# Optimization experiments

Measured on AMD Instinct MI355X. Metric: run time of the kernel, lower is better.

The kernel has to match this reference:

```python
import jax, jax.numpy as jnp
import numpy as np

B, C, L = 4, 512, 4096
H = 8
DH = C // H
MLP = 2048


def _ln(x, g, b, eps=1e-5):
    mu = x.mean(-1, keepdims=True)
    var = ((x - mu) ** 2).mean(-1, keepdims=True)
    return (x - mu) / jnp.sqrt(var + eps) * g + b


def setup_inputs() -> dict:
    key = jax.random.key(0)
    ks = jax.random.split(key, 16)
    s = 0.02
    d = {
        "x": jax.random.normal(ks[0], (B, C, L), jnp.float32),
        "Wq": jax.random.normal(ks[1], (C, C), jnp.float32) * s,
        "bq": jnp.zeros((C,), jnp.float32),
        "gq": jnp.ones((C,), jnp.float32),
        "betaq": jnp.zeros((C,), jnp.float32),
        "Wk": jax.random.normal(ks[2], (C, C), jnp.float32) * s,
        "bk": jnp.zeros((C,), jnp.float32),
        "gk": jnp.ones((C,), jnp.float32),
        "betak": jnp.zeros((C,), jnp.float32),
        "Wv": jax.random.normal(ks[3], (C, C), jnp.float32) * s,
        "bv": jnp.zeros((C,), jnp.float32),
        "gv": jnp.ones((C,), jnp.float32),
        "betav": jnp.zeros((C,), jnp.float32),
        "Wkq": jax.random.normal(ks[4], (C, C), jnp.float32) * s,
        "bkq": jnp.zeros((C,), jnp.float32),
        "Wkk": jax.random.normal(ks[5], (C, C), jnp.float32) * s,
        "bkk": jnp.zeros((C,), jnp.float32),
        "g_attn": jnp.ones((C,), jnp.float32),
        "b_attn": jnp.zeros((C,), jnp.float32),
        "W1": jax.random.normal(ks[6], (C, MLP), jnp.float32) * s,
        "b1": jnp.zeros((MLP,), jnp.float32),
        "W2": jax.random.normal(ks[7], (MLP, C), jnp.float32) * s,
        "b2": jnp.zeros((C,), jnp.float32),
    }
    return d


def _split_heads(t):
    # [B, L, C] -> [B, H, L, DH]
    b, l, _ = t.shape
    return t.reshape(b, l, H, DH).transpose(0, 2, 1, 3)


def reference(x, Wq, bq, gq, betaq, Wk, bk, gk, betak, Wv, bv, gv, betav,
              Wkq, bkq, Wkk, bkk, g_attn, b_attn, W1, b1, W2, b2):
    # x: [B, C, L] -> flatten(2).permute(0,2,1) -> [B, L, C]
    xf = jnp.transpose(x, (0, 2, 1))
    Q = _ln(xf @ Wq + bq, gq, betaq)            # [B, L, C]
    K = _ln(xf @ Wk + bk, gk, betak)            # [B, L, C]
    V = _ln(xf @ Wv + bv, gv, betav)            # [B, L, C]
    # add zero token to K, V (seq dim)
    z = jnp.zeros((x.shape[0], 1, C), x.dtype)
    K = jnp.concatenate([z, K], axis=1)         # [B, Lk, C], Lk = L+1
    V = jnp.concatenate([z, V], axis=1)
    phiQ = jnp.tanh(Q @ Wkq + bkq) + 1.0        # [B, L, C]
    phiK = jnp.tanh(K @ Wkk + bkk) + 1.0        # [B, Lk, C]

    Qh, Kh, Vh = _split_heads(Q), _split_heads(K), _split_heads(V)
    pQ, pK = _split_heads(phiQ), _split_heads(phiK)  # [B,H,L,DH], [B,H,Lk,DH]

    # softmax-reweighted phi_K: score from mean-query probe against K
    q_probe = Qh.mean(axis=2)                                   # [B,H,DH]
    score = jnp.einsum('bhd,bhld->bhl', q_probe, Kh) / jnp.sqrt(jnp.float32(DH))
    score = jax.nn.softmax(score, axis=-1)                      # [B,H,Lk]
    pKw = pK * score[..., None]                                 # [B,H,Lk,DH]

    kv = jnp.einsum('bhld,bhle->bhde', pKw, Vh)                 # [B,H,DH,DH]
    num = jnp.einsum('bhqd,bhde->bhqe', pQ, kv)                 # [B,H,L,DH]
    ksum = pKw.sum(axis=2)                                      # [B,H,DH]
    bottom = jnp.einsum('bhqd,bhd->bhq', pQ, ksum)[..., None] + 1e-6
    out_h = num / bottom                                        # [B,H,L,DH]

    out = out_h.transpose(0, 2, 1, 3).reshape(x.shape[0], -1, C)  # [B,L,C]
    a = _ln(out, g_attn, b_attn)
    m = jax.nn.gelu(a @ W1 + b1, approximate=False) @ W2 + b2
    res = a + m                                                 # residual MLP
    res = jnp.transpose(res, (0, 2, 1))                         # [B,C,L]
    return res + x
```

## Files before the change

kernel.cpp:

```cpp
#include <hip/hip_runtime.h>
#include <math.h>

#define B_ 4
#define C_ 512
#define L_ 4096
#define H_ 8
#define DH_ 64
#define MLP_ 2048
#define BL_ (B_*L_)
#define LK_ (L_+1)

typedef _Float16 f16;
typedef _Float16 f16x8 __attribute__((ext_vector_type(8)));
typedef _Float16 f16x4 __attribute__((ext_vector_type(4)));
typedef float f32x4 __attribute__((ext_vector_type(4)));

__device__ __forceinline__ void gl16(void* lds, const void* g) {
  __builtin_amdgcn_global_load_lds((const __attribute__((address_space(1))) void*)g,
                                   (__attribute__((address_space(3))) void*)lds,
                                   16, 0, 0);
}

__device__ __forceinline__ float frcp(float x) { return __builtin_amdgcn_rcpf(x); }

__global__ __launch_bounds__(256) void transpose_w(const float* __restrict__ W,
                                                   f16* __restrict__ Wt, int K, int N) {
  __shared__ float tile[32][33];
  int n0 = blockIdx.x * 32, k0 = blockIdx.y * 32;
  int tx = threadIdx.x & 31, ty = threadIdx.x >> 5;
#pragma unroll
  for (int i = 0; i < 4; ++i)
    tile[ty + i * 8][tx] = W[(size_t)(k0 + ty + i * 8) * N + n0 + tx];
  __syncthreads();
#pragma unroll
  for (int i = 0; i < 4; ++i)
    Wt[(size_t)(n0 + ty + i * 8) * K + k0 + tx] = (f16)tile[tx][ty + i * 8];
}

__global__ __launch_bounds__(256) void transpose_x(const float* __restrict__ x,
                                                   f16* __restrict__ xf) {
  __shared__ float tile[32][33];
  int b = blockIdx.z;
  int l0 = blockIdx.x * 32, c0 = blockIdx.y * 32;
  int tx = threadIdx.x & 31, ty = threadIdx.x >> 5;
#pragma unroll
  for (int i = 0; i < 4; ++i)
    tile[ty + i * 8][tx] = x[((size_t)b * C_ + c0 + ty + i * 8) * L_ + l0 + tx];
  __syncthreads();
#pragma unroll
  for (int i = 0; i < 4; ++i)
    xf[((size_t)b * L_ + l0 + ty + i * 8) * C_ + c0 + tx] = (f16)tile[tx][ty + i * 8];
}

__global__ __launch_bounds__(256) void final_add(const f16* __restrict__ a,
                                                 const f16* __restrict__ m,
                                                 const float* __restrict__ x,
                                                 float* __restrict__ out) {
  __shared__ float tile[32][33];
  int b = blockIdx.z;
  int l0 = blockIdx.x * 32, c0 = blockIdx.y * 32;
  int tx = threadIdx.x & 31, ty = threadIdx.x >> 5;
#pragma unroll
  for (int i = 0; i < 4; ++i) {
    size_t idx = ((size_t)b * L_ + l0 + ty + i * 8) * C_ + c0 + tx;
    tile[ty + i * 8][tx] = (float)a[idx] + (float)m[idx];
  }
  __syncthreads();
#pragma unroll
  for (int i = 0; i < 4; ++i) {
    size_t o = ((size_t)b * C_ + c0 + ty + i * 8) * L_ + l0 + tx;
    out[o] = tile[tx][ty + i * 8] + x[o];
  }
}

__global__ __launch_bounds__(256) void pack_params(
    const float* bq, const float* bk, const float* bv,
    const float* gq, const float* gk, const float* gv,
    const float* betaq, const float* betak, const float* betav,
    const float* bkq, const float* bkk,
    float* bqkv, float* gqkv, float* betaqkv, float* bphi) {
  int i = blockIdx.x * 256 + threadIdx.x;
  int w = i >> 9, c = i & 511;
  bqkv[i]    = (w == 0 ? bq : (w == 1 ? bk : bv))[c];
  gqkv[i]    = (w == 0 ? gq : (w == 1 ? gk : gv))[c];
  betaqkv[i] = (w == 0 ? betaq : (w == 1 ? betak : betav))[c];
  if (i < 1024) bphi[i] = (i < 512) ? bkq[i] : bkk[i - 512];
}

template <int EPI>
__global__ __launch_bounds__(256) void gemm64(const f16* __restrict__ A,
                                              const f16* __restrict__ Bt,
                                              const float* __restrict__ bias,
                                              f16* __restrict__ Ch,
                                              int N, int K,
                                              const float* __restrict__ Bot,
                                              long long zA, long long zB,
                                              long long zC, long long zBias,
                                              long long zBot) {
  __shared__ f16 smem[2 * 128 * 64];
  f16* As = smem;
  f16* Bs = smem + 128 * 64;
  A  += (size_t)blockIdx.z * zA;
  Bt += (size_t)blockIdx.z * zB;
  Ch += (size_t)blockIdx.z * zC;
  if (EPI == 3) Bot += (size_t)blockIdx.z * zBot;
  else          bias += (size_t)blockIdx.z * zBias;

  const int tid = threadIdx.x;
  const int lane = tid & 63, wv = tid >> 6;
  const int wm = wv >> 1, wn = wv & 1;
  const int bm = blockIdx.x * 128, bn = blockIdx.y * 128;
  const int l15 = lane & 15, q = lane >> 4;

  const int srow = tid >> 3;
  const int schunk = (tid & 7) ^ (srow & 7);
  const f16* pa = A + (size_t)(bm + srow) * K + schunk * 8;
  const f16* pb = Bt + (size_t)(bn + srow) * K + schunk * 8;
  f16* la = As + tid * 8;
  f16* lb = Bs + tid * 8;
  const int sw0 = (q ^ (lane & 7)) * 8;
  const int sw1 = ((4 + q) ^ (lane & 7)) * 8;

  f32x4 acc[4][4] = {};

  for (int k0 = 0; k0 < K; k0 += 64) {
    __syncthreads();
#pragma unroll
    for (int p = 0; p < 4; ++p) gl16(la + p * 2048, pa + (size_t)p * 32 * K + k0);
#pragma unroll
    for (int p = 0; p < 4; ++p) gl16(lb + p * 2048, pb + (size_t)p * 32 * K + k0);
    __syncthreads();
#pragma unroll
    for (int ks = 0; ks < 2; ++ks) {
      const int sw = ks ? sw1 : sw0;
      f16x8 af[4], bf[4];
#pragma unroll
      for (int i = 0; i < 4; ++i)
        af[i] = *(const f16x8*)&As[(wm * 64 + i * 16 + l15) * 64 + sw];
#pragma unroll
      for (int j = 0; j < 4; ++j)
        bf[j] = *(const f16x8*)&Bs[(wn * 64 + j * 16 + l15) * 64 + sw];
#pragma unroll
      for (int i = 0; i < 4; ++i)
#pragma unroll
        for (int j = 0; j < 4; ++j)
          acc[i][j] = __builtin_amdgcn_mfma_f32_16x16x32_f16(af[i], bf[j], acc[i][j], 0, 0, 0);
    }
  }

  __syncthreads();
#pragma unroll
  for (int j = 0; j < 4; ++j) {
    int lc = wn * 64 + j * 16 + l15;
    float bb = (EPI == 3) ? 0.f : bias[bn + lc];
#pragma unroll
    for (int i = 0; i < 4; ++i) {
#pragma unroll
      for (int r = 0; r < 4; ++r) {
        int lr = wm * 64 + i * 16 + q * 4 + r;
        float v = acc[i][j][r] + bb;
        if (EPI == 1) {
          v = 2.0f * frcp(1.0f + __expf(-2.0f * v));
        } else if (EPI == 2) {
          v = v * frcp(1.0f + __expf(-1.5957691f * (v + 0.044715f * v * v * v)));
        } else if (EPI == 3) {
          v = v * frcp(Bot[(size_t)(bm + lr) * H_ + ((bn + lc) >> 6)] + 1e-6f);
        }
        smem[lr * 128 + ((((lc >> 3) ^ (lr & 15)) << 3) | (lc & 7))] = (f16)v;
      }
    }
  }
  __syncthreads();
#pragma unroll
  for (int p = 0; p < 8; ++p) {
    int idx = p * 256 + tid;
    int row = idx >> 4, ch = idx & 15;
    f16x8 vv = *(const f16x8*)&smem[row * 128 + ((ch ^ (row & 15)) << 3)];
    *(f16x8*)&Ch[(size_t)(bm + row) * N + bn + ch * 8] = vv;
  }
}

__global__ __launch_bounds__(256) void ln16(const f16* __restrict__ X,
                                            const float* __restrict__ g,
                                            const float* __restrict__ bta,
                                            f16* __restrict__ Y, int threeway) {
  int wv = threadIdx.x >> 6, lane = threadIdx.x & 63;
  int r = blockIdx.x * 4 + wv;
  int token = r, which = 0;
  if (threeway) { token = r / 3; which = r - token * 3; }
  const f16* xr = X + (size_t)r * C_;
  f16x8 v = *(const f16x8*)(xr + lane * 8);
  float vals[8];
  float s = 0.f, s2 = 0.f;
#pragma unroll
  for (int j = 0; j < 8; ++j) { vals[j] = (float)v[j]; s += vals[j]; s2 += vals[j] * vals[j]; }
#pragma unroll
  for (int m_ = 1; m_ < 64; m_ <<= 1) { s += __shfl_xor(s, m_); s2 += __shfl_xor(s2, m_); }
  float mu = s * (1.f / C_);
  float var = s2 * (1.f / C_) - mu * mu;
  float rstd = rsqrtf(var + 1e-5f);
  const float* gp = g + which * C_;
  const float* bp = bta + which * C_;
  f16x8 o;
#pragma unroll
  for (int j = 0; j < 8; ++j) {
    int c = lane * 8 + j;
    o[j] = (f16)((vals[j] - mu) * rstd * gp[c] + bp[c]);
  }
  *(f16x8*)(Y + ((size_t)which * BL_ + token) * C_ + lane * 8) = o;
}

__global__ __launch_bounds__(256) void qprobe2(const f16* __restrict__ Q,
                                               float* __restrict__ qp) {
  int blk = blockIdx.x;
  int b = blk >> 6;
  int r0 = blk * 64;
  int t = threadIdx.x;
  int c8 = (t & 63) * 8, rg = t >> 6;
  float s[8] = {0.f, 0.f, 0.f, 0.f, 0.f, 0.f, 0.f, 0.f};
#pragma unroll
  for (int i = 0; i < 16; ++i) {
    const f16* row = Q + ((size_t)r0 + rg + i * 4) * C_ + c8;
    f16x8 v = *(const f16x8*)row;
#pragma unroll
    for (int j = 0; j < 8; ++j) s[j] += (float)v[j];
  }
  __shared__ float red[4][520];
#pragma unroll
  for (int j = 0; j < 8; ++j) red[rg][c8 + j] = s[j];
  __syncthreads();
  int c = t * 2;
  float a0 = red[0][c] + red[1][c] + red[2][c] + red[3][c];
  float a1 = red[0][c + 1] + red[1][c + 1] + red[2][c + 1] + red[3][c + 1];
  atomicAdd(&qp[b * C_ + c], a0);
  atomicAdd(&qp[b * C_ + c + 1], a1);
}

__global__ __launch_bounds__(256) void logits_kernel(const f16* __restrict__ Kh,
                                                     const float* __restrict__ qp,
                                                     float* __restrict__ score) {
  int wv = threadIdx.x >> 6, lane = threadIdx.x & 63;
  int token = blockIdx.x * 4 + wv;
  int b = token >> 12;
  int l = token & (L_ - 1);
  const f16* row = Kh + (size_t)token * C_;
  int h = lane >> 3, j0 = (lane & 7) * 8;
  const float* qph = qp + b * C_ + h * DH_ + j0;
  float p = 0.f;
#pragma unroll
  for (int j = 0; j < 8; ++j) p += qph[j] * (float)row[h * DH_ + j0 + j];
  p += __shfl_xor(p, 1); p += __shfl_xor(p, 2); p += __shfl_xor(p, 4);
  if ((lane & 7) == 0)
    score[((size_t)b * H_ + h) * LK_ + 1 + l] = p * (1.f / L_) * 0.125f;
}

__global__ __launch_bounds__(256) void softmax_kernel(float* __restrict__ score) {
  int bh = blockIdx.x, t = threadIdx.x;
  float* s = score + (size_t)bh * LK_;
  __shared__ float red[256];
  float mx = 0.f;
  for (int i = t; i < L_; i += 256) mx = fmaxf(mx, s[1 + i]);
  red[t] = mx; __syncthreads();
  for (int k = 128; k; k >>= 1) { if (t < k) red[t] = fmaxf(red[t], red[t + k]); __syncthreads(); }
  mx = red[0]; __syncthreads();
  float sum = (t == 0) ? expf(-mx) : 0.f;
  for (int i = t; i < L_; i += 256) { float e = expf(s[1 + i] - mx); s[1 + i] = e; sum += e; }
  red[t] = sum; __syncthreads();
  for (int k = 128; k; k >>= 1) { if (t < k) red[t] += red[t + k]; __syncthreads(); }
  float inv = 1.f / red[0];
  __syncthreads();
  for (int i = t; i < L_; i += 256) s[1 + i] *= inv;
  if (t == 0) s[0] = expf(-mx) * inv;
}

__global__ __launch_bounds__(256) void ksum_init(const float* __restrict__ score,
                                                 const float* __restrict__ bkk,
                                                 float* __restrict__ ksum) {
  int i = blockIdx.x * 256 + threadIdx.x;
  int bh = i >> 6, d = i & 63, h = bh & 7;
  float pk0 = tanhf(bkk[h * DH_ + d]) + 1.f;
  ksum[i] = score[(size_t)bh * LK_] * pk0;
}

#define PIDX(l, c) ((l) * 68 + (c))
#define AIDX(d, e) ((d) * 68 + (e) + ((((d) >> 3)) << 2))
__global__ __launch_bounds__(256, 2) void kv_part_kernel(const f16* __restrict__ phiK,
                                                         const f16* __restrict__ Vh,
                                                         const float* __restrict__ score,
                                                         float* __restrict__ kvp,
                                                         float* __restrict__ ksum) {
  __shared__ float sm0[4416];
  __shared__ float sm1[4416];
  int bh = blockIdx.y, b = bh >> 3, h = bh & 7;
  int part = blockIdx.x;
  int l0 = part * 256;
  int t = threadIdx.x, lane = t & 63, wv = t >> 6;
  int R = (lane >> 3) * 8, Cc = (lane & 7) * 8;
  float acc[8][8] = {};
  float ks[8] = {0.f, 0.f, 0.f, 0.f, 0.f, 0.f, 0.f, 0.f};

  for (int c = 0; c < 4; ++c) {
    int lc = l0 + c * 64;
    __syncthreads();
#pragma unroll
    for (int p = 0; p < 4; ++p) {
      int l = p * 16 + (t >> 4);
      int c4 = (t & 15) * 4;
      size_t grow = ((size_t)b * L_ + lc + l) * C_ + h * DH_ + c4;
      float w = score[(size_t)bh * LK_ + 1 + lc + l];
      f16x4 pk = *(const f16x4*)(phiK + grow);
      f16x4 vvv = *(const f16x4*)(Vh + grow);
      sm0[PIDX(l, c4) + 0] = w * (float)pk[0];
      sm0[PIDX(l, c4) + 1] = w * (float)pk[1];
      sm0[PIDX(l, c4) + 2] = w * (float)pk[2];
      sm0[PIDX(l, c4) + 3] = w * (float)pk[3];
      sm1[PIDX(l, c4) + 0] = (float)vvv[0];
      sm1[PIDX(l, c4) + 1] = (float)vvv[1];
      sm1[PIDX(l, c4) + 2] = (float)vvv[2];
      sm1[PIDX(l, c4) + 3] = (float)vvv[3];
    }
    __syncthreads();
#pragma unroll
    for (int i = 0; i < 16; ++i) {
      int ll = wv * 16 + i;
      float4 a0 = *(const float4*)&sm0[PIDX(ll, R)];
      float4 a1 = *(const float4*)&sm0[PIDX(ll, R + 4)];
      float4 b0 = *(const float4*)&sm1[PIDX(ll, Cc)];
      float4 b1 = *(const float4*)&sm1[PIDX(ll, Cc + 4)];
      float av[8] = {a0.x, a0.y, a0.z, a0.w, a1.x, a1.y, a1.z, a1.w};
      float bv2[8] = {b0.x, b0.y, b0.z, b0.w, b1.x, b1.y, b1.z, b1.w};
#pragma unroll
      for (int ii = 0; ii < 8; ++ii)
#pragma unroll
        for (int jj = 0; jj < 8; ++jj) acc[ii][jj] += av[ii] * bv2[jj];
      if ((lane & 7) == 0) {
#pragma unroll
        for (int ii = 0; ii < 8; ++ii) ks[ii] += av[ii];
      }
    }
  }

  __syncthreads();
  if ((lane & 7) == 0) {
#pragma unroll
    for (int i = 0; i < 8; ++i) sm1[wv * 64 + R + i] = ks[i];
  }
  for (int w = 0; w < 4; ++w) {
    if (wv == w) {
#pragma unroll
      for (int i = 0; i < 8; ++i) {
        float* p0 = &sm0[AIDX(R + i, Cc)];
        if (w == 0) {
          *(float4*)p0 = make_float4(acc[i][0], acc[i][1], acc[i][2], acc[i][3]);
          *(float4*)(p0 + 4) = make_float4(acc[i][4], acc[i][5], acc[i][6], acc[i][7]);
        } else {
          float4 o0 = *(const float4*)p0, o1 = *(const float4*)(p0 + 4);
          o0.x += acc[i][0]; o0.y += acc[i][1]; o0.z += acc[i][2]; o0.w += acc[i][3];
          o1.x += acc[i][4]; o1.y += acc[i][5]; o1.z += acc[i][6]; o1.w += acc[i][7];
          *(float4*)p0 = o0;
          *(float4*)(p0 + 4) = o1;
        }
      }
    }
    __syncthreads();
  }
  if (t < 64) {
    float s = sm1[t] + sm1[64 + t] + sm1[128 + t] + sm1[192 + t];
    atomicAdd(&ksum[bh * 64 + t], s);
  }
  float* dst = kvp + ((size_t)bh * 16 + part) * 4096;
#pragma unroll
  for (int i = 0; i < 16; ++i) {
    int idx = i * 256 + t;
    dst[idx] = sm0[AIDX(idx & 63, idx >> 6)];
  }
}

__global__ __launch_bounds__(256) void build_bd(const float* __restrict__ kvp,
                                                f16* __restrict__ BD) {
  size_t i = (size_t)blockIdx.x * 256 + threadIdx.x;
  int b = (int)(i >> 18);
  int nk = (int)(i & 262143);
  int n = nk >> 9, k = nk & 511;
  int hn = n >> 6, hk = k >> 6;
  float v = 0.f;
  if (hn == hk) {
    const float* p = kvp + ((size_t)(b * H_ + hn) * 16) * 4096 + (n & 63) * 64 + (k & 63);
#pragma unroll
    for (int pp = 0; pp < 16; ++pp) v += p[pp * 4096];
  }
  BD[i] = (f16)v;
}

__global__ __launch_bounds__(256) void bottom_kernel(const f16* __restrict__ phiQ,
                                                     const float* __restrict__ ksum,
                                                     float* __restrict__ bot) {
  int wv = threadIdx.x >> 6, lane = threadIdx.x & 63;
  int token = blockIdx.x * 4 + wv;
  int b = token >> 12;
  const f16* row = phiQ + (size_t)token * C_;
  int h = lane >> 3, j0 = (lane & 7) * 8;
  const float* ks = ksum + (b * H_ + h) * 64 + j0;
  float p = 0.f;
#pragma unroll
  for (int j = 0; j < 8; ++j) p += ks[j] * (float)row[h * DH_ + j0 + j];
  p += __shfl_xor(p, 1); p += __shfl_xor(p, 2); p += __shfl_xor(p, 4);
  if ((lane & 7) == 0) bot[(size_t)token * H_ + h] = p;
}

extern "C" void kernel_launch(void* const* d_in, const int* in_sizes, int n_in,
                              void* d_out, int out_size, void* d_ws, size_t ws_size,
                              hipStream_t stream) {
  (void)in_sizes; (void)n_in; (void)out_size; (void)ws_size;
  const float* x     = (const float*)d_in[0];
  const float* Wq    = (const float*)d_in[1];
  const float* bq    = (const float*)d_in[2];
  const float* gq    = (const float*)d_in[3];
  const float* betaq = (const float*)d_in[4];
  const float* Wk    = (const float*)d_in[5];
  const float* bk    = (const float*)d_in[6];
  const float* gk    = (const float*)d_in[7];
  const float* betak = (const float*)d_in[8];
  const float* Wv    = (const float*)d_in[9];
  const float* bv    = (const float*)d_in[10];
  const float* gv    = (const float*)d_in[11];
  const float* betav = (const float*)d_in[12];
  const float* Wkq   = (const float*)d_in[13];
  const float* bkq   = (const float*)d_in[14];
  const float* Wkk   = (const float*)d_in[15];
  const float* bkk   = (const float*)d_in[16];
  const float* g_at  = (const float*)d_in[17];
  const float* b_at  = (const float*)d_in[18];
  const float* W1    = (const float*)d_in[19];
  const float* b1    = (const float*)d_in[20];
  const float* W2    = (const float*)d_in[21];
  const float* b2    = (const float*)d_in[22];
  float* out = (float*)d_out;

  char* ws = (char*)d_ws;
  size_t off = 0;
  auto alloc = [&](size_t bytes) -> void* {
    void* p = ws + off;
    off += (bytes + 255) & ~(size_t)255;
    return p;
  };
  f16* U1    = (f16*)alloc((size_t)BL_ * MLP_ * 2);
  f16* QKVh  = (f16*)alloc((size_t)3 * BL_ * C_ * 2);
  f16* phiQK = (f16*)alloc((size_t)2 * BL_ * C_ * 2);
  f16* xf    = (f16*)alloc((size_t)BL_ * C_ * 2);
  f16* WqkvT = (f16*)alloc((size_t)3 * C_ * C_ * 2);
  f16* WkqT  = (f16*)alloc((size_t)C_ * C_ * 2);
  f16* WkkT  = (f16*)alloc((size_t)C_ * C_ * 2);
  f16* W1T   = (f16*)alloc((size_t)C_ * MLP_ * 2);
  f16* W2T   = (f16*)alloc((size_t)MLP_ * C_ * 2);
  f16* BD    = (f16*)alloc((size_t)B_ * C_ * C_ * 2);
  float* score = (float*)alloc((size_t)B_ * H_ * LK_ * 4);
  float* qp    = (float*)alloc((size_t)B_ * C_ * 4);
  float* kvp   = (float*)alloc((size_t)B_ * H_ * 16 * 4096 * 4);
  float* ksum  = (float*)alloc((size_t)B_ * H_ * DH_ * 4);
  float* bot   = (float*)alloc((size_t)BL_ * H_ * 4);
  float* bqkv    = (float*)alloc(1536 * 4);
  float* gqkv    = (float*)alloc(1536 * 4);
  float* betaqkv = (float*)alloc(1536 * 4);
  float* bphi    = (float*)alloc(1024 * 4);

  f16* tmpqkv = U1;
  f16* tmpA   = U1;
  f16* h1     = U1;
  f16* Qh = QKVh;
  f16* Kh = QKVh + (size_t)BL_ * C_;
  f16* Vh = QKVh + (size_t)2 * BL_ * C_;
  f16* ah = QKVh;
  f16* phiQ = phiQK;
  f16* phiK = phiQK + (size_t)BL_ * C_;
  f16* mbuf = phiQK;

  dim3 blk(256);

  pack_params<<<6, blk, 0, stream>>>(bq, bk, bv, gq, gk, gv, betaq, betak, betav,
                                     bkq, bkk, bqkv, gqkv, betaqkv, bphi);

  transpose_w<<<dim3(C_ / 32, C_ / 32), blk, 0, stream>>>(Wq, WqkvT, C_, C_);
  transpose_w<<<dim3(C_ / 32, C_ / 32), blk, 0, stream>>>(Wk, WqkvT + (size_t)C_ * C_, C_, C_);
  transpose_w<<<dim3(C_ / 32, C_ / 32), blk, 0, stream>>>(Wv, WqkvT + (size_t)2 * C_ * C_, C_, C_);
  transpose_w<<<dim3(C_ / 32, C_ / 32), blk, 0, stream>>>(Wkq, WkqT, C_, C_);
  transpose_w<<<dim3(C_ / 32, C_ / 32), blk, 0, stream>>>(Wkk, WkkT, C_, C_);
  transpose_w<<<dim3(MLP_ / 32, C_ / 32), blk, 0, stream>>>(W1, W1T, C_, MLP_);
  transpose_w<<<dim3(C_ / 32, MLP_ / 32), blk, 0, stream>>>(W2, W2T, MLP_, C_);

  transpose_x<<<dim3(L_ / 32, C_ / 32, B_), blk, 0, stream>>>(x, xf);

  gemm64<5><<<dim3(BL_ / 128, 1536 / 128), blk, 0, stream>>>(
      xf, WqkvT, bqkv, tmpqkv, 1536, C_, nullptr, 0, 0, 0, 0, 0);
  ln16<<<3 * BL_ / 4, blk, 0, stream>>>(tmpqkv, gqkv, betaqkv, QKVh, 1);

  hipMemsetAsync(qp, 0, (size_t)B_ * C_ * 4, stream);
  qprobe2<<<BL_ / 64, blk, 0, stream>>>(Qh, qp);

  gemm64<1><<<dim3(BL_ / 128, C_ / 128, 2), blk, 0, stream>>>(
      Qh, WkqT, bphi, phiQ, C_, C_, nullptr,
      (long long)BL_ * C_, (long long)C_ * C_, (long long)BL_ * C_, (long long)C_, 0);

  logits_kernel<<<BL_ / 4, blk, 0, stream>>>(Kh, qp, score);
  softmax_kernel<<<B_ * H_, blk, 0, stream>>>(score);

  ksum_init<<<(B_ * H_ * DH_) / 256, blk, 0, stream>>>(score, bkk, ksum);
  kv_part_kernel<<<dim3(16, B_ * H_), blk, 0, stream>>>(phiK, Vh, score, kvp, ksum);

  build_bd<<<(B_ * C_ * C_) / 256, blk, 0, stream>>>(kvp, BD);
  bottom_kernel<<<BL_ / 4, blk, 0, stream>>>(phiQ, ksum, bot);

  gemm64<3><<<dim3(L_ / 128, C_ / 128, B_), blk, 0, stream>>>(
      phiQ, BD, nullptr, tmpA, C_, C_, bot,
      (long long)L_ * C_, (long long)C_ * C_, (long long)L_ * C_, 0, (long long)L_ * H_);

  ln16<<<BL_ / 4, blk, 0, stream>>>(tmpA, g_at, b_at, ah, 0);

  gemm64<2><<<dim3(BL_ / 128, MLP_ / 128), blk, 0, stream>>>(
      ah, W1T, b1, h1, MLP_, C_, nullptr, 0, 0, 0, 0, 0);
  gemm64<5><<<dim3(BL_ / 128, C_ / 128), blk, 0, stream>>>(
      h1, W2T, b2, mbuf, C_, MLP_, nullptr, 0, 0, 0, 0, 0);

  final_add<<<dim3(L_ / 32, C_ / 32, B_), blk, 0, stream>>>(ah, mbuf, x, out);
}
```

Measured before the change: 437.5 us.

## Double-buffer GEMM LDS loads, fuse residual+transpose into last GEMM, merge weight transposes

The GEMM now double-buffers its LDS tiles, so global loads for the next K-step are issued before the MFMAs on the current step and one barrier per iteration is dropped. LDS use grows to 64KB per block and launch bounds request 2 blocks per CU. The final residual add and the transpose back to [B,C,L] are folded into the W2 GEMM epilogue, which removes the separate final_add kernel and the f16 mbuf round trip. The five square weight transposes are merged into one launch. The prefetch issued into the other buffer relies on the single top-of-loop barrier for correctness, which is a race risk.

New measurement: 408.4 us. 1.07x faster.

```diff
diff --git a/kernel.cpp b/kernel.cpp
--- a/kernel.cpp
+++ b/kernel.cpp
@@ -23,6 +23,27 @@
 
 __device__ __forceinline__ float frcp(float x) { return __builtin_amdgcn_rcpf(x); }
 
+__global__ __launch_bounds__(256) void transpose_w5(const float* __restrict__ Wq,
+                                                    const float* __restrict__ Wk,
+                                                    const float* __restrict__ Wv,
+                                                    const float* __restrict__ Wkq,
+                                                    const float* __restrict__ Wkk,
+                                                    f16* __restrict__ dst) {
+  int z = blockIdx.z;
+  const float* W = (z == 0) ? Wq : (z == 1) ? Wk : (z == 2) ? Wv : (z == 3) ? Wkq : Wkk;
+  f16* Wt = dst + (size_t)z * C_ * C_;
+  __shared__ float tile[32][33];
+  int n0 = blockIdx.x * 32, k0 = blockIdx.y * 32;
+  int tx = threadIdx.x & 31, ty = threadIdx.x >> 5;
+#pragma unroll
+  for (int i = 0; i < 4; ++i)
+    tile[ty + i * 8][tx] = W[(size_t)(k0 + ty + i * 8) * C_ + n0 + tx];
+  __syncthreads();
+#pragma unroll
+  for (int i = 0; i < 4; ++i)
+    Wt[(size_t)(n0 + ty + i * 8) * C_ + k0 + tx] = (f16)tile[tx][ty + i * 8];
+}
+
 __global__ __launch_bounds__(256) void transpose_w(const float* __restrict__ W,
                                                    f16* __restrict__ Wt, int K, int N) {
   __shared__ float tile[32][33];
@@ -50,27 +71,6 @@
 #pragma unroll
   for (int i = 0; i < 4; ++i)
     xf[((size_t)b * L_ + l0 + ty + i * 8) * C_ + c0 + tx] = (f16)tile[tx][ty + i * 8];
-}
-
-__global__ __launch_bounds__(256) void final_add(const f16* __restrict__ a,
-                                                 const f16* __restrict__ m,
-                                                 const float* __restrict__ x,
-                                                 float* __restrict__ out) {
-  __shared__ float tile[32][33];
-  int b = blockIdx.z;
-  int l0 = blockIdx.x * 32, c0 = blockIdx.y * 32;
-  int tx = threadIdx.x & 31, ty = threadIdx.x >> 5;
-#pragma unroll
-  for (int i = 0; i < 4; ++i) {
-    size_t idx = ((size_t)b * L_ + l0 + ty + i * 8) * C_ + c0 + tx;
-    tile[ty + i * 8][tx] = (float)a[idx] + (float)m[idx];
-  }
-  __syncthreads();
-#pragma unroll
-  for (int i = 0; i < 4; ++i) {
-    size_t o = ((size_t)b * C_ + c0 + ty + i * 8) * L_ + l0 + tx;
-    out[o] = tile[tx][ty + i * 8] + x[o];
-  }
 }
 
 __global__ __launch_bounds__(256) void pack_params(
@@ -88,21 +88,22 @@
 }
 
 template <int EPI>
-__global__ __launch_bounds__(256) void gemm64(const f16* __restrict__ A,
-                                              const f16* __restrict__ Bt,
-                                              const float* __restrict__ bias,
-                                              f16* __restrict__ Ch,
-                                              int N, int K,
-                                              const float* __restrict__ Bot,
-                                              long long zA, long long zB,
-                                              long long zC, long long zBias,
-                                              long long zBot) {
-  __shared__ f16 smem[2 * 128 * 64];
-  f16* As = smem;
-  f16* Bs = smem + 128 * 64;
+__global__ __launch_bounds__(256, 2) void gemm64(const f16* __restrict__ A,
+                                                 const f16* __restrict__ Bt,
+                                                 const float* __restrict__ bias,
+                                                 f16* __restrict__ Ch,
+                                                 int N, int K,
+                                                 const float* __restrict__ Bot,
+                                                 const f16* __restrict__ Ares,
+                                                 const float* __restrict__ Xres,
+                                                 float* __restrict__ Fout,
+                                                 long long zA, long long zB,
+                                                 long long zC, long long zBias,
+                                                 long long zBot) {
+  __shared__ f16 smem[2 * 128 * 128];
   A  += (size_t)blockIdx.z * zA;
   Bt += (size_t)blockIdx.z * zB;
-  Ch += (size_t)blockIdx.z * zC;
+  if (EPI != 6) Ch += (size_t)blockIdx.z * zC;
   if (EPI == 3) Bot += (size_t)blockIdx.z * zBot;
   else          bias += (size_t)blockIdx.z * zBias;
 
@@ -116,20 +117,30 @@
   const int schunk = (tid & 7) ^ (srow & 7);
   const f16* pa = A + (size_t)(bm + srow) * K + schunk * 8;
   const f16* pb = Bt + (size_t)(bn + srow) * K + schunk * 8;
-  f16* la = As + tid * 8;
-  f16* lb = Bs + tid * 8;
+  f16* la = smem + tid * 8;
+  f16* lb = smem + 8192 + tid * 8;
   const int sw0 = (q ^ (lane & 7)) * 8;
   const int sw1 = ((4 + q) ^ (lane & 7)) * 8;
 
   f32x4 acc[4][4] = {};
 
+#pragma unroll
+  for (int p = 0; p < 4; ++p) gl16(la + p * 2048, pa + (size_t)p * 32 * K);
+#pragma unroll
+  for (int p = 0; p < 4; ++p) gl16(lb + p * 2048, pb + (size_t)p * 32 * K);
+
+  int cur = 0;
   for (int k0 = 0; k0 < K; k0 += 64) {
     __syncthreads();
-#pragma unroll
-    for (int p = 0; p < 4; ++p) gl16(la + p * 2048, pa + (size_t)p * 32 * K + k0);
-#pragma unroll
-    for (int p = 0; p < 4; ++p) gl16(lb + p * 2048, pb + (size_t)p * 32 * K + k0);
-    __syncthreads();
+    const int nxt = cur ^ 1;
+    if (k0 + 64 < K) {
+#pragma unroll
+      for (int p = 0; p < 4; ++p) gl16(la + nxt * 16384 + p * 2048, pa + (size_t)p * 32 * K + k0 + 64);
+#pragma unroll
+      for (int p = 0; p < 4; ++p) gl16(lb + nxt * 16384 + p * 2048, pb + (size_t)p * 32 * K + k0 + 64);
+    }
+    const f16* As = smem + cur * 16384;
+    const f16* Bs = As + 8192;
 #pragma unroll
     for (int ks = 0; ks < 2; ++ks) {
       const int sw = ks ? sw1 : sw0;
@@ -146,6 +157,7 @@
         for (int j = 0; j < 4; ++j)
           acc[i][j] = __builtin_amdgcn_mfma_f32_16x16x32_f16(af[i], bf[j], acc[i][j], 0, 0, 0);
     }
+    cur = nxt;
   }
 
   __syncthreads();
@@ -171,12 +183,44 @@
     }
   }
   __syncthreads();
-#pragma unroll
-  for (int p = 0; p < 8; ++p) {
-    int idx = p * 256 + tid;
-    int row = idx >> 4, ch = idx & 15;
-    f16x8 vv = *(const f16x8*)&smem[row * 128 + ((ch ^ (row & 15)) << 3)];
-    *(f16x8*)&Ch[(size_t)(bm + row) * N + bn + ch * 8] = vv;
+
+  if (EPI != 6) {
+#pragma unroll
+    for (int p = 0; p < 8; ++p) {
+      int idx = p * 256 + tid;
+      int row = idx >> 4, ch = idx & 15;
+      f16x8 vv = *(const f16x8*)&smem[row * 128 + ((ch ^ (row & 15)) << 3)];
+      *(f16x8*)&Ch[(size_t)(bm + row) * N + bn + ch * 8] = vv;
+    }
+  } else {
+#pragma unroll
+    for (int p = 0; p < 8; ++p) {
+      int idx = p * 256 + tid;
+      int row = idx >> 4, ch = idx & 15;
+      f16x8 av = *(const f16x8*)&Ares[(size_t)(bm + row) * C_ + bn + ch * 8];
+      f16* sp = &smem[row * 128 + ((ch ^ (row & 15)) << 3)];
+      f16x8 sv = *(const f16x8*)sp;
+#pragma unroll
+      for (int jj = 0; jj < 8; ++jj) sv[jj] = (f16)((float)sv[jj] + (float)av[jj]);
+      *(f16x8*)sp = sv;
+    }
+    __syncthreads();
+    int c = tid & 127, lh = tid >> 7;
+    int b = bm >> 12, lbase = (bm & 4095) + lh * 64;
+    const float* xp = Xres + ((size_t)b * C_ + bn + c) * L_ + lbase;
+    float* op = Fout + ((size_t)b * C_ + bn + c) * L_ + lbase;
+    int chi = c >> 3, clo = c & 7;
+#pragma unroll
+    for (int s = 0; s < 16; ++s) {
+      int l = lh * 64 + s * 4;
+      float4 xv = *(const float4*)(xp + s * 4);
+      float4 r;
+      r.x = (float)smem[(l + 0) * 128 + (((chi ^ ((l + 0) & 15)) << 3) | clo)] + xv.x;
+      r.y = (float)smem[(l + 1) * 128 + (((chi ^ ((l + 1) & 15)) << 3) | clo)] + xv.y;
+      r.z = (float)smem[(l + 2) * 128 + (((chi ^ ((l + 2) & 15)) << 3) | clo)] + xv.z;
+      r.w = (float)smem[(l + 3) * 128 + (((chi ^ ((l + 3) & 15)) << 3) | clo)] + xv.w;
+      *(float4*)(op + s * 4) = r;
+    }
   }
 }
 
@@ -473,32 +517,27 @@
   f16* ah = QKVh;
   f16* phiQ = phiQK;
   f16* phiK = phiQK + (size_t)BL_ * C_;
-  f16* mbuf = phiQK;
 
   dim3 blk(256);
 
   pack_params<<<6, blk, 0, stream>>>(bq, bk, bv, gq, gk, gv, betaq, betak, betav,
                                      bkq, bkk, bqkv, gqkv, betaqkv, bphi);
 
-  transpose_w<<<dim3(C_ / 32, C_ / 32), blk, 0, stream>>>(Wq, WqkvT, C_, C_);
-  transpose_w<<<dim3(C_ / 32, C_ / 32), blk, 0, stream>>>(Wk, WqkvT + (size_t)C_ * C_, C_, C_);
-  transpose_w<<<dim3(C_ / 32, C_ / 32), blk, 0, stream>>>(Wv, WqkvT + (size_t)2 * C_ * C_, C_, C_);
-  transpose_w<<<dim3(C_ / 32, C_ / 32), blk, 0, stream>>>(Wkq, WkqT, C_, C_);
-  transpose_w<<<dim3(C_ / 32, C_ / 32), blk, 0, stream>>>(Wkk, WkkT, C_, C_);
+  transpose_w5<<<dim3(16, 16, 5), blk, 0, stream>>>(Wq, Wk, Wv, Wkq, Wkk, WqkvT);
   transpose_w<<<dim3(MLP_ / 32, C_ / 32), blk, 0, stream>>>(W1, W1T, C_, MLP_);
   transpose_w<<<dim3(C_ / 32, MLP_ / 32), blk, 0, stream>>>(W2, W2T, MLP_, C_);
 
   transpose_x<<<dim3(L_ / 32, C_ / 32, B_), blk, 0, stream>>>(x, xf);
 
   gemm64<5><<<dim3(BL_ / 128, 1536 / 128), blk, 0, stream>>>(
-      xf, WqkvT, bqkv, tmpqkv, 1536, C_, nullptr, 0, 0, 0, 0, 0);
+      xf, WqkvT, bqkv, tmpqkv, 1536, C_, nullptr, nullptr, nullptr, nullptr, 0, 0, 0, 0, 0);
   ln16<<<3 * BL_ / 4, blk, 0, stream>>>(tmpqkv, gqkv, betaqkv, QKVh, 1);
 
   hipMemsetAsync(qp, 0, (size_t)B_ * C_ * 4, stream);
   qprobe2<<<BL_ / 64, blk, 0, stream>>>(Qh, qp);
 
   gemm64<1><<<dim3(BL_ / 128, C_ / 128, 2), blk, 0, stream>>>(
-      Qh, WkqT, bphi, phiQ, C_, C_, nullptr,
+      Qh, WkqT, bphi, phiQ, C_, C_, nullptr, nullptr, nullptr, nullptr,
       (long long)BL_ * C_, (long long)C_ * C_, (long long)BL_ * C_, (long long)C_, 0);
 
   logits_kernel<<<BL_ / 4, blk, 0, stream>>>(Kh, qp, score);
@@ -511,15 +550,13 @@
   bottom_kernel<<<BL_ / 4, blk, 0, stream>>>(phiQ, ksum, bot);
 
   gemm64<3><<<dim3(L_ / 128, C_ / 128, B_), blk, 0, stream>>>(
-      phiQ, BD, nullptr, tmpA, C_, C_, bot,
+      phiQ, BD, nullptr, tmpA, C_, C_, bot, nullptr, nullptr, nullptr,
       (long long)L_ * C_, (long long)C_ * C_, (long long)L_ * C_, 0, (long long)L_ * H_);
 
   ln16<<<BL_ / 4, blk, 0, stream>>>(tmpA, g_at, b_at, ah, 0);
 
   gemm64<2><<<dim3(BL_ / 128, MLP_ / 128), blk, 0, stream>>>(
-      ah, W1T, b1, h1, MLP_, C_, nullptr, 0, 0, 0, 0, 0);
-  gemm64<5><<<dim3(BL_ / 128, C_ / 128), blk, 0, stream>>>(
-      h1, W2T, b2, mbuf, C_, MLP_, nullptr, 0, 0, 0, 0, 0);
-
-  final_add<<<dim3(L_ / 32, C_ / 32, B_), blk, 0, stream>>>(ah, mbuf, x, out);
-}
+      ah, W1T, b1, h1, MLP_, C_, nullptr, nullptr, nullptr, nullptr, 0, 0, 0, 0, 0);
+  gemm64<6><<<dim3(BL_ / 128, C_ / 128), blk, 0, stream>>>(
+      h1, W2T, b2, nullptr, C_, MLP_, nullptr, ah, x, out, 0, 0, 0, 0, 0);
+}
```
